# Optimization experiments

Hardware: AMD Instinct MI355X
Metric: run time of the kernel (lower is better)

## Reference

```python
import jax, jax.numpy as jnp
import numpy as np

B, S, D, H = 2, 2048, 512, 8
DH = D // H


def layer_norm(x, w, b, eps=1e-5):
    mu = x.mean(-1, keepdims=True)
    var = x.var(-1, keepdims=True)  # biased, matches nn.LayerNorm
    return (x - mu) / jnp.sqrt(var + eps) * w + b


def map_norm(qk, eps=1e-5):
    # torch.var default is unbiased (ddof=1)
    mu = qk.mean(-1, keepdims=True)
    var = qk.var(-1, ddof=1, keepdims=True)
    return (qk - mu) / jnp.sqrt(var + eps)


def sinmax(x):
    s = 1.0 + jnp.sin(10.0 * x)
    return s / s.sum(-1, keepdims=True)


def setup_inputs() -> dict:
    key = jax.random.key(0)
    ks = jax.random.split(key, 8)
    sc = 0.02
    return {
        "x": jax.random.normal(ks[0], (B, S, D), jnp.float32),
        "norm_w": jnp.ones((D,), jnp.float32),
        "norm_b": jnp.zeros((D,), jnp.float32),
        "qvk_w": jax.random.normal(ks[1], (D, 3 * D), jnp.float32) * sc,
        "qvk_b": jnp.zeros((3 * D,), jnp.float32),
        "concat_w": jax.random.normal(ks[2], (D, D), jnp.float32) * sc,
        "concat_b": jnp.zeros((D,), jnp.float32),
        "mlp_norm_w": jnp.ones((D,), jnp.float32),
        "mlp_norm_b": jnp.zeros((D,), jnp.float32),
        "mlp1_w": jax.random.normal(ks[3], (D, 2 * D), jnp.float32) * sc,
        "mlp1_b": jnp.zeros((2 * D,), jnp.float32),
        "mlp2_w": jax.random.normal(ks[4], (2 * D, D), jnp.float32) * sc,
        "mlp2_b": jnp.zeros((D,), jnp.float32),
    }


def reference(x, norm_w, norm_b, qvk_w, qvk_b, concat_w, concat_b,
              mlp_norm_w, mlp_norm_b, mlp1_w, mlp1_b, mlp2_w, mlp2_b):
    res = x
    xn = layer_norm(x, norm_w, norm_b)
    qvk = jax.nn.relu(xn @ qvk_w + qvk_b)                      # [B,S,3D]
    Q, K, V = qvk[..., :D], qvk[..., D:2 * D], qvk[..., 2 * D:]
    # contiguous d_per_head chunks per head == reshape to [B,S,H,DH]
    q = Q.reshape(B, S, H, DH).transpose(0, 2, 1, 3)           # [B,H,S,DH]
    k = K.reshape(B, S, H, DH).transpose(0, 2, 1, 3)
    v = V.reshape(B, S, H, DH).transpose(0, 2, 1, 3)
    qk = jnp.einsum('bhqd,bhkd->bhqk', q, k)                   # [B,H,S,S]
    qk = map_norm(qk)                                          # norm_ variant
    scores = sinmax(qk / np.sqrt(DH))                          # sinmax variant
    hv = jnp.einsum('bhqk,bhkd->bhqd', scores, v)
    attout = hv.transpose(0, 2, 1, 3).reshape(B, S, D)
    attout = attout @ concat_w + concat_b + res
    res_mlp = attout
    a = layer_norm(attout, mlp_norm_w, mlp_norm_b)
    h = jax.nn.gelu(a @ mlp1_w + mlp1_b, approximate=False)
    mlpout = h @ mlp2_w + mlp2_b
    return (mlpout + res_mlp, scores)
```

## Files before the change

### kernel.cpp

```cpp
#include <hip/hip_runtime.h>

#define Bb_ 2
#define S_ 2048
#define D_ 512
#define H_ 8
#define DH_ 64

typedef __attribute__((ext_vector_type(8))) __bf16 bf16x8;
typedef __attribute__((ext_vector_type(4))) __bf16 bf16x4;
typedef __attribute__((ext_vector_type(2))) __bf16 bf16x2;
typedef __attribute__((ext_vector_type(4))) float f32x4;
typedef __attribute__((ext_vector_type(8))) short short8;
typedef __attribute__((ext_vector_type(4))) unsigned u32x4;
typedef __attribute__((ext_vector_type(2))) unsigned u32x2;

__device__ __forceinline__ void gload_lds16(const void* g, void* l) {
  __builtin_amdgcn_global_load_lds(
      (const __attribute__((address_space(1))) unsigned int*)g,
      (__attribute__((address_space(3))) unsigned int*)l, 16, 0, 0);
}

__global__ __launch_bounds__(256) void wtrans_all(
    const float* __restrict__ qvk_w, const float* __restrict__ concat_w,
    const float* __restrict__ mlp1_w, const float* __restrict__ mlp2_w,
    __bf16* __restrict__ qvk_wT, __bf16* __restrict__ concat_wT,
    __bf16* __restrict__ mlp1_wT, __bf16* __restrict__ mlp2_wT) {
  int b = blockIdx.x;
  const float* w;
  __bf16* wt;
  int K, N, idx0;
  if (b < 3072) { w = qvk_w; wt = qvk_wT; K = 512; N = 1536; idx0 = b * 256; }
  else if (b < 4096) { w = concat_w; wt = concat_wT; K = 512; N = 512; idx0 = (b - 3072) * 256; }
  else if (b < 6144) { w = mlp1_w; wt = mlp1_wT; K = 512; N = 1024; idx0 = (b - 4096) * 256; }
  else { w = mlp2_w; wt = mlp2_wT; K = 1024; N = 512; idx0 = (b - 6144) * 256; }
  int idx = idx0 + threadIdx.x;
  int k = idx / N, n = idx - k * N;
  wt[(long)n * K + k] = (__bf16)w[idx];
}

__global__ __launch_bounds__(256) void ln_kernel(const float* __restrict__ x,
                                                 const float* __restrict__ w,
                                                 const float* __restrict__ b,
                                                 __bf16* __restrict__ out) {
  long row = blockIdx.x;
  const float* xr = x + row * 512;
  int t = threadIdx.x;
  float2 v = *reinterpret_cast<const float2*>(xr + t * 2);
  float s = v.x + v.y;
  float sq = v.x * v.x + v.y * v.y;
#pragma unroll
  for (int m = 1; m < 64; m <<= 1) {
    s += __shfl_xor(s, m);
    sq += __shfl_xor(sq, m);
  }
  __shared__ float red[8];
  int wid = t >> 6;
  if ((t & 63) == 0) { red[wid] = s; red[wid + 4] = sq; }
  __syncthreads();
  s = red[0] + red[1] + red[2] + red[3];
  sq = red[4] + red[5] + red[6] + red[7];
  float mu = s * (1.f / 512.f);
  float var = sq * (1.f / 512.f) - mu * mu;
  float rs = rsqrtf(var + 1e-5f);
  int c = t * 2;
  float o0 = (v.x - mu) * rs * w[c] + b[c];
  float o1 = (v.y - mu) * rs * w[c + 1] + b[c + 1];
  bf16x2 ov;
  ov[0] = (__bf16)o0;
  ov[1] = (__bf16)o1;
  *reinterpret_cast<bf16x2*>(out + row * 512 + c) = ov;
}

template <int ACT, int OUTMODE, bool HASRES>
__global__ __launch_bounds__(256) void gemm_kernel(
    const __bf16* __restrict__ A, const __bf16* __restrict__ Bt,
    const float* __restrict__ bias, const float* __restrict__ res,
    float* __restrict__ outF, __bf16* __restrict__ outB,
    __bf16* __restrict__ outK, __bf16* __restrict__ outVt,
    int lda, int ldb, int ldc, int K) {
  __shared__ __align__(16) __bf16 smem[128 * 128];
  __bf16* As = smem;
  __bf16* Bs = smem + 128 * 64;
  int t = threadIdx.x, lane = t & 63, wid = t >> 6;
  const __bf16* Ab = A + (long)blockIdx.y * 128 * lda;
  const __bf16* Bb = Bt + (long)blockIdx.x * 128 * ldb;

  f32x4 acc[4][4];
#pragma unroll
  for (int i = 0; i < 4; i++)
#pragma unroll
    for (int j = 0; j < 4; j++) acc[i][j] = (f32x4){0.f, 0.f, 0.f, 0.f};

  int wr = wid >> 1, wc = wid & 1;
  int kq = lane >> 4;
  int cbase = wid * 256;

  for (int k0 = 0; k0 < K; k0 += 64) {
    __syncthreads();
#pragma unroll
    for (int j = 0; j < 4; j++) {
      int ci = cbase + j * 64 + lane;
      int row = ci >> 3;
      int c = ci & 7;
      int sc = c ^ (row & 7);
      gload_lds16(Ab + (long)row * lda + k0 + sc * 8, &As[(cbase + j * 64) * 8]);
      gload_lds16(Bb + (long)row * ldb + k0 + sc * 8, &Bs[(cbase + j * 64) * 8]);
    }
    __syncthreads();
#pragma unroll
    for (int ks = 0; ks < 2; ks++) {
      bf16x8 af[4], bfr[4];
#pragma unroll
      for (int fm = 0; fm < 4; fm++) {
        int r = wr * 64 + fm * 16 + (lane & 15);
        int c = (ks * 4 + kq) ^ (r & 7);
        af[fm] = *reinterpret_cast<const bf16x8*>(&As[r * 64 + c * 8]);
      }
#pragma unroll
      for (int fn = 0; fn < 4; fn++) {
        int r = wc * 64 + fn * 16 + (lane & 15);
        int c = (ks * 4 + kq) ^ (r & 7);
        bfr[fn] = *reinterpret_cast<const bf16x8*>(&Bs[r * 64 + c * 8]);
      }
#pragma unroll
      for (int fm = 0; fm < 4; fm++)
#pragma unroll
        for (int fn = 0; fn < 4; fn++)
          acc[fm][fn] = __builtin_amdgcn_mfma_f32_16x16x32_bf16(af[fm], bfr[fn],
                                                                acc[fm][fn], 0, 0, 0);
    }
  }

  if (OUTMODE == 2) {
    __syncthreads();
    char* Cb = reinterpret_cast<char*>(smem);
#pragma unroll
    for (int fm = 0; fm < 4; fm++)
#pragma unroll
      for (int fn = 0; fn < 4; fn++) {
        int c = wc * 64 + fn * 16 + (lane & 15);
        int gcol = blockIdx.x * 128 + c;
        float bv = bias[gcol];
#pragma unroll
        for (int r4 = 0; r4 < 4; r4++) {
          int r = wr * 64 + fm * 16 + kq * 4 + r4;
          float v = fmaxf(acc[fm][fn][r4] + bv, 0.f);
          *reinterpret_cast<__bf16*>(Cb + r * 256 + (((c >> 3) ^ (r & 7)) << 4) +
                                     ((c & 7) << 1)) = (__bf16)v;
        }
      }
    __syncthreads();
    long bbq = (blockIdx.y * 128) >> 11;
    int srow0 = (blockIdx.y * 128) & 2047;
    if (blockIdx.x < 8) {
      int r = t >> 1, half = t & 1;
      int gcol = blockIdx.x * 128 + half * 64;
      __bf16* dst;
      if (gcol < 512)
        dst = outB + ((bbq * 8 + (gcol >> 6)) * 2048 + srow0 + r) * 64;
      else
        dst = outK + ((bbq * 8 + ((gcol - 512) >> 6)) * 2048 + srow0 + r) * 64;
      const char* srcrow = Cb + r * 256;
#pragma unroll
      for (int j = 0; j < 8; j++) {
        bf16x8 vv = *reinterpret_cast<const bf16x8*>(
            srcrow + ((((half * 8 + j) ^ (r & 7))) << 4));
        *reinterpret_cast<bf16x8*>(dst + j * 8) = vv;
      }
    } else {
      int d = t & 63, seg = t >> 6;
      int srow = srow0 + seg * 32;
#pragma unroll
      for (int h2 = 0; h2 < 2; h2++) {
        int c = h2 * 64 + d;
        int h = (blockIdx.x * 128 - 1024 + h2 * 64) >> 6;
        __bf16* dst = outVt + (bbq * 8 + h) * 131072 + (srow >> 5) * 2048 + d * 32;
        bf16x8 wv8[4];
#pragma unroll
        for (int i = 0; i < 32; i++) {
          int r = seg * 32 + i;
          __bf16 val = *reinterpret_cast<const __bf16*>(
              Cb + r * 256 + (((c >> 3) ^ (r & 7)) << 4) + ((c & 7) << 1));
          wv8[i >> 3][i & 7] = val;
        }
#pragma unroll
        for (int i4 = 0; i4 < 4; i4++)
          *reinterpret_cast<bf16x8*>(dst + i4 * 8) = wv8[i4];
      }
    }
    return;
  }

  long gr0 = (long)blockIdx.y * 128 + wr * 64;
  long gc0 = (long)blockIdx.x * 128 + wc * 64;
#pragma unroll
  for (int fm = 0; fm < 4; fm++)
#pragma unroll
    for (int fn = 0; fn < 4; fn++) {
      int col = (int)gc0 + fn * 16 + (lane & 15);
      long rbase = gr0 + fm * 16 + kq * 4;
      float bv = bias ? bias[col] : 0.f;
#pragma unroll
      for (int r4 = 0; r4 < 4; r4++) {
        long grow = rbase + r4;
        float v = acc[fm][fn][r4] + bv;
        if (HASRES) v += res[grow * ldc + col];
        if (ACT == 1) v = fmaxf(v, 0.f);
        if (ACT == 2) v = 0.5f * v * (1.f + erff(v * 0.70710678118f));
        if (OUTMODE == 0) {
          outF[grow * ldc + col] = v;
        } else {
          outB[grow * ldc + col] = (__bf16)v;
        }
      }
    }
}

__global__ __launch_bounds__(256) void gram_kernel(const __bf16* __restrict__ Kh,
                                                   float* __restrict__ gpart,
                                                   float* __restrict__ kpart) {
  int head = blockIdx.x >> 5, chunk = blockIdx.x & 31;
  __shared__ __align__(16) __bf16 kl[64 * 64];
  int t = threadIdx.x;
  const __bf16* src = Kh + ((long)head * 2048 + chunk * 64) * 64;
#pragma unroll
  for (int i = 0; i < 2; i++) {
    int e = (i * 256 + t) * 8;
    *reinterpret_cast<short8*>(&kl[e]) = *reinterpret_cast<const short8*>(&src[e]);
  }
  __syncthreads();
  int d1 = t & 63, g = t >> 6;
  float acc[16];
#pragma unroll
  for (int i = 0; i < 16; i++) acc[i] = 0.f;
  float kb = 0.f;
  for (int r = 0; r < 64; r++) {
    float k1 = (float)kl[r * 64 + d1];
    kb += k1;
    bf16x8 a = *reinterpret_cast<const bf16x8*>(&kl[r * 64 + g * 16]);
    bf16x8 b = *reinterpret_cast<const bf16x8*>(&kl[r * 64 + g * 16 + 8]);
#pragma unroll
    for (int i = 0; i < 8; i++) acc[i] += k1 * (float)a[i];
#pragma unroll
    for (int i = 0; i < 8; i++) acc[8 + i] += k1 * (float)b[i];
  }
  float* gp = gpart + ((long)chunk * 16 + head) * 4096 + d1 * 64 + g * 16;
#pragma unroll
  for (int i = 0; i < 16; i++) gp[i] = acc[i];
  if (g == 0) kpart[(chunk * 16 + head) * 64 + d1] = kb;
}

__global__ __launch_bounds__(256) void greduce_kernel(const float* __restrict__ gpart,
                                                      const float* __restrict__ kpart,
                                                      float* __restrict__ G,
                                                      float* __restrict__ kbar) {
  int idx = blockIdx.x * 256 + threadIdx.x;
  if (idx < 65536) {
    int head = idx >> 12, e = idx & 4095;
    float s = 0.f;
#pragma unroll 4
    for (int c = 0; c < 32; c++) s += gpart[((long)c * 16 + head) * 4096 + e];
    G[idx] = s;
  } else if (idx < 66560) {
    int k = idx - 65536;
    int head = k >> 6, d = k & 63;
    float s = 0.f;
#pragma unroll 4
    for (int c = 0; c < 32; c++) s += kpart[(c * 16 + head) * 64 + d];
    kbar[k] = s * (1.f / 2048.f);
  }
}

__global__ __launch_bounds__(256, 4) void stats_kernel(const __bf16* __restrict__ Qh,
                                                       const float* __restrict__ G,
                                                       const float* __restrict__ kbar,
                                                       float2* __restrict__ stats) {
  int head = blockIdx.x >> 5, sub = blockIdx.x & 31;
  __shared__ float Gl[4096];
  __shared__ float kbl[64];
  __shared__ __align__(16) float qlf[64 * 68];
  int t = threadIdx.x;
  const float* Gsrc = G + head * 4096;
#pragma unroll
  for (int i = 0; i < 4; i++) {
    int e = (i * 256 + t) * 4;
    *reinterpret_cast<float4*>(&Gl[e]) = *reinterpret_cast<const float4*>(&Gsrc[e]);
  }
  if (t < 16)
    *reinterpret_cast<float4*>(&kbl[t * 4]) =
        *reinterpret_cast<const float4*>(&kbar[head * 64 + t * 4]);
  const __bf16* qsrc = Qh + ((long)head * 2048 + sub * 64) * 64;
#pragma unroll
  for (int i = 0; i < 2; i++) {
    int e = (i * 256 + t) * 8;
    bf16x8 v = *reinterpret_cast<const bf16x8*>(&qsrc[e]);
    int row = e >> 6, col = e & 63;
    float* dst = &qlf[row * 68 + col];
#pragma unroll
    for (int j = 0; j < 8; j++) dst[j] = (float)v[j];
  }
  __syncthreads();
  int qrow = t >> 2, qt = t & 3;
  const float* qr = &qlf[qrow * 68];
  float mup = 0.f, s2p = 0.f;
#pragma unroll
  for (int i = 0; i < 16; i++) {
    int d1 = qt * 16 + i;
    const float* Gr = &Gl[d1 * 64];
    float acc = 0.f;
#pragma unroll
    for (int j = 0; j < 64; j++) acc += Gr[j] * qr[j];
    float q1 = qr[d1];
    s2p += q1 * acc;
    mup += q1 * kbl[d1];
  }
  mup += __shfl_xor(mup, 1); mup += __shfl_xor(mup, 2);
  s2p += __shfl_xor(s2p, 1); s2p += __shfl_xor(s2p, 2);
  if (qt == 0) {
    float mu = mup;
    float var = (s2p - 2048.f * mu * mu) * (1.f / 2047.f);
    stats[(head << 11) + sub * 64 + qrow] = make_float2(mu, rsqrtf(var + 1e-5f));
  }
}

__global__ __launch_bounds__(256) void attn6_kernel(
    const __bf16* __restrict__ Qh, const __bf16* __restrict__ Kh,
    const __bf16* __restrict__ Vp, const float2* __restrict__ stats,
    float* __restrict__ sco, __bf16* __restrict__ hv) {
  __shared__ __align__(16) __bf16 Ks[128 * 64];
  __shared__ __align__(16) __bf16 Vs[4 * 64 * 32];

  int bid = blockIdx.x;
  int xcd = bid & 7, j = bid >> 3;
  int head = xcd * 2 + (j >> 5);
  int qt = j & 31;
  int bb = head >> 3, hh = head & 7;
  int q0 = qt * 64;

  int t = threadIdx.x, lane = t & 63, wv = t >> 6;
  int cg = lane >> 4, ln = lane & 15;
  int sw7 = ln & 7, sw3 = ln & 3;

  int qrow = q0 + wv * 16 + ln;
  const __bf16* Qr = Qh + ((long)head * 2048 + qrow) * 64;
  bf16x8 qf0 = *reinterpret_cast<const bf16x8*>(Qr + cg * 8);
  bf16x8 qf1 = *reinterpret_cast<const bf16x8*>(Qr + 32 + cg * 8);
  float2 st = stats[(head << 11) + qrow];
  float mu = st.x, rs = st.y;

  const __bf16* Kbase = Kh + (long)head * 131072;
  const __bf16* Vbase = Vp + (long)head * 131072;

  float Z = 0.f;
  for (int kt = 0; kt < 16; kt++) {
    __syncthreads();
    const __bf16* Kt = Kbase + kt * 8192;
#pragma unroll
    for (int jj = 0; jj < 4; jj++) {
      int ci = wv * 256 + jj * 64 + lane;
      int row = ci >> 3, c = ci & 7, sc = c ^ (row & 7);
      gload_lds16(Kt + row * 64 + sc * 8, &Ks[(wv * 256 + jj * 64) * 8]);
    }
    __syncthreads();
#pragma unroll
    for (int sl = 0; sl < 8; sl++) {
      const __bf16* kr = &Ks[(sl * 16 + ln) * 64];
      bf16x8 a0 = *reinterpret_cast<const bf16x8*>(kr + ((cg ^ sw7) * 8));
      bf16x8 a1 = *reinterpret_cast<const bf16x8*>(kr + (((cg + 4) ^ sw7) * 8));
      f32x4 d = (f32x4){0.f, 0.f, 0.f, 0.f};
      d = __builtin_amdgcn_mfma_f32_16x16x32_bf16(a0, qf0, d, 0, 0, 0);
      d = __builtin_amdgcn_mfma_f32_16x16x32_bf16(a1, qf1, d, 0, 0, 0);
      Z += (1.f + __sinf(1.25f * (d[0] - mu) * rs));
      Z += (1.f + __sinf(1.25f * (d[1] - mu) * rs));
      Z += (1.f + __sinf(1.25f * (d[2] - mu) * rs));
      Z += (1.f + __sinf(1.25f * (d[3] - mu) * rs));
    }
  }
  Z += __shfl_xor(Z, 16);
  Z += __shfl_xor(Z, 32);
  float invZ = 1.f / Z;

  f32x4 hacc[4];
#pragma unroll
  for (int dt = 0; dt < 4; dt++) hacc[dt] = (f32x4){0.f, 0.f, 0.f, 0.f};
  float* srow = sco + ((long)head * 2048 + qrow) * 2048;

  for (int kt = 0; kt < 16; kt++) {
    __syncthreads();
    const __bf16* Kt = Kbase + kt * 8192;
    const __bf16* Vt = Vbase + kt * 8192;
#pragma unroll
    for (int jj = 0; jj < 4; jj++) {
      int ci = wv * 256 + jj * 64 + lane;
      int rowk = ci >> 3, ck = ci & 7, sck = ck ^ (rowk & 7);
      gload_lds16(Kt + rowk * 64 + sck * 8, &Ks[(wv * 256 + jj * 64) * 8]);
      int rowv = ci >> 2, cv = ci & 3, scv = cv ^ (rowv & 3);
      gload_lds16(Vt + rowv * 32 + scv * 8, &Vs[(wv * 256 + jj * 64) * 8]);
    }
    __syncthreads();
#pragma unroll
    for (int w = 0; w < 4; w++) {
      const __bf16* kr0 = &Ks[(w * 32 + ln) * 64];
      const __bf16* kr1 = &Ks[(w * 32 + 16 + ln) * 64];
      f32x4 d0 = (f32x4){0.f, 0.f, 0.f, 0.f}, d1 = (f32x4){0.f, 0.f, 0.f, 0.f};
      d0 = __builtin_amdgcn_mfma_f32_16x16x32_bf16(
          *reinterpret_cast<const bf16x8*>(kr0 + ((cg ^ sw7) * 8)), qf0, d0, 0, 0, 0);
      d0 = __builtin_amdgcn_mfma_f32_16x16x32_bf16(
          *reinterpret_cast<const bf16x8*>(kr0 + (((cg + 4) ^ sw7) * 8)), qf1, d0, 0, 0, 0);
      d1 = __builtin_amdgcn_mfma_f32_16x16x32_bf16(
          *reinterpret_cast<const bf16x8*>(kr1 + ((cg ^ sw7) * 8)), qf0, d1, 0, 0, 0);
      d1 = __builtin_amdgcn_mfma_f32_16x16x32_bf16(
          *reinterpret_cast<const bf16x8*>(kr1 + (((cg + 4) ^ sw7) * 8)), qf1, d1, 0, 0, 0);
      float p0 = 1.f + __sinf(1.25f * (d0[0] - mu) * rs);
      float p1 = 1.f + __sinf(1.25f * (d0[1] - mu) * rs);
      float p2 = 1.f + __sinf(1.25f * (d0[2] - mu) * rs);
      float p3 = 1.f + __sinf(1.25f * (d0[3] - mu) * rs);
      float p4 = 1.f + __sinf(1.25f * (d1[0] - mu) * rs);
      float p5 = 1.f + __sinf(1.25f * (d1[1] - mu) * rs);
      float p6 = 1.f + __sinf(1.25f * (d1[2] - mu) * rs);
      float p7 = 1.f + __sinf(1.25f * (d1[3] - mu) * rs);
      f32x4 o0 = (f32x4){p0 * invZ, p1 * invZ, p2 * invZ, p3 * invZ};
      f32x4 o1 = (f32x4){p4 * invZ, p5 * invZ, p6 * invZ, p7 * invZ};
      *reinterpret_cast<f32x4*>(srow + kt * 128 + w * 32 + cg * 4) = o0;
      *reinterpret_cast<f32x4*>(srow + kt * 128 + w * 32 + 16 + cg * 4) = o1;
      bf16x2 c0, c1, c2, c3;
      c0[0] = (__bf16)p0; c0[1] = (__bf16)p1;
      c1[0] = (__bf16)p2; c1[1] = (__bf16)p3;
      c2[0] = (__bf16)p4; c2[1] = (__bf16)p5;
      c3[0] = (__bf16)p6; c3[1] = (__bf16)p7;
      u32x4 pk = (u32x4){__builtin_bit_cast(unsigned, c0), __builtin_bit_cast(unsigned, c1),
                         __builtin_bit_cast(unsigned, c2), __builtin_bit_cast(unsigned, c3)};
      bf16x8 pf = __builtin_bit_cast(bf16x8, pk);
#pragma unroll
      for (int dt = 0; dt < 4; dt++) {
        const char* vr = reinterpret_cast<const char*>(Vs) + (w * 64 + dt * 16 + ln) * 64;
        int b0 = ((((cg >> 1) ^ sw3)) << 4) + ((cg & 1) << 3);
        int b1 = (((((cg >> 1) + 2) ^ sw3)) << 4) + ((cg & 1) << 3);
        u32x2 vlo = *reinterpret_cast<const u32x2*>(vr + b0);
        u32x2 vhi = *reinterpret_cast<const u32x2*>(vr + b1);
        u32x4 vpk = (u32x4){vlo[0], vlo[1], vhi[0], vhi[1]};
        bf16x8 vf = __builtin_bit_cast(bf16x8, vpk);
        hacc[dt] = __builtin_amdgcn_mfma_f32_16x16x32_bf16(vf, pf, hacc[dt], 0, 0, 0);
      }
    }
  }

  {
    __bf16* hq = hv + ((long)(bb * 2048) + qrow) * 512 + hh * 64;
#pragma unroll
    for (int dt = 0; dt < 4; dt++) {
      bf16x2 w0, w1;
      w0[0] = (__bf16)(hacc[dt][0] * invZ);
      w0[1] = (__bf16)(hacc[dt][1] * invZ);
      w1[0] = (__bf16)(hacc[dt][2] * invZ);
      w1[1] = (__bf16)(hacc[dt][3] * invZ);
      *reinterpret_cast<bf16x2*>(hq + dt * 16 + cg * 4) = w0;
      *reinterpret_cast<bf16x2*>(hq + dt * 16 + cg * 4 + 2) = w1;
    }
  }
}

extern "C" void kernel_launch(void* const* d_in, const int* in_sizes, int n_in,
                              void* d_out, int out_size, void* d_ws, size_t ws_size,
                              hipStream_t stream) {
  const float* x = (const float*)d_in[0];
  const float* norm_w = (const float*)d_in[1];
  const float* norm_b = (const float*)d_in[2];
  const float* qvk_w = (const float*)d_in[3];
  const float* qvk_b = (const float*)d_in[4];
  const float* concat_w = (const float*)d_in[5];
  const float* concat_b = (const float*)d_in[6];
  const float* mlp_norm_w = (const float*)d_in[7];
  const float* mlp_norm_b = (const float*)d_in[8];
  const float* mlp1_w = (const float*)d_in[9];
  const float* mlp1_b = (const float*)d_in[10];
  const float* mlp2_w = (const float*)d_in[11];
  const float* mlp2_b = (const float*)d_in[12];

  char* ws = (char*)d_ws;
  __bf16* qvk_wT = (__bf16*)(ws + 0);
  __bf16* concat_wT = (__bf16*)(ws + 1572864);
  __bf16* mlp1_wT = (__bf16*)(ws + 2097152);
  __bf16* mlp2_wT = (__bf16*)(ws + 3145728);
  __bf16* xn = (__bf16*)(ws + 4194304);
  __bf16* Qh = (__bf16*)(ws + 8388608);
  __bf16* Kh = (__bf16*)(ws + 12582912);
  __bf16* Vp = (__bf16*)(ws + 16777216);
  __bf16* hv = (__bf16*)(ws + 20971520);
  float* gpart = (float*)(ws + 25165824);
  float* attout = (float*)(ws + 25165824);
  float* kpart = (float*)(ws + 33554432);
  float* G = (float*)(ws + 33685504);
  float* kbar = (float*)(ws + 33947648);
  float2* stats = (float2*)(ws + 33951744);
  __bf16* a_b = (__bf16*)(ws + 33554432);
  __bf16* h_b = (__bf16*)(ws + 37748736);

  float* out0 = (float*)d_out;
  float* sco = out0 + 2097152;

  wtrans_all<<<8192, 256, 0, stream>>>(qvk_w, concat_w, mlp1_w, mlp2_w,
                                       qvk_wT, concat_wT, mlp1_wT, mlp2_wT);

  ln_kernel<<<4096, 256, 0, stream>>>(x, norm_w, norm_b, xn);

  gemm_kernel<1, 2, false><<<dim3(12, 32), 256, 0, stream>>>(
      xn, qvk_wT, qvk_b, nullptr, nullptr, Qh, Kh, Vp, 512, 512, 1536, 512);

  gram_kernel<<<512, 256, 0, stream>>>(Kh, gpart, kpart);
  greduce_kernel<<<260, 256, 0, stream>>>(gpart, kpart, G, kbar);
  stats_kernel<<<512, 256, 0, stream>>>(Qh, G, kbar, stats);

  attn6_kernel<<<512, 256, 0, stream>>>(Qh, Kh, Vp, stats, sco, hv);

  gemm_kernel<0, 0, true><<<dim3(4, 32), 256, 0, stream>>>(
      hv, concat_wT, concat_b, x, attout, nullptr, nullptr, nullptr, 512, 512, 512, 512);

  ln_kernel<<<4096, 256, 0, stream>>>(attout, mlp_norm_w, mlp_norm_b, a_b);

  gemm_kernel<2, 1, false><<<dim3(8, 32), 256, 0, stream>>>(
      a_b, mlp1_wT, mlp1_b, nullptr, nullptr, h_b, nullptr, nullptr, 512, 512, 1024, 512);

  gemm_kernel<0, 0, true><<<dim3(4, 32), 256, 0, stream>>>(
      h_b, mlp2_wT, mlp2_b, attout, out0, nullptr, nullptr, nullptr, 1024, 1024, 512, 1024);
}
```

Measured before the change: 222.2 us.

## Tile weight transpose through LDS and halve GEMM row tile for small GEMMs

The weight transpose/convert kernel now stages 64x64 tiles in shared memory, reading float4 rows and writing bf16x8 columns, instead of one strided scalar store per thread. The concat, MLP1 and MLP2 GEMMs are templated on a 64-row tile with a 1x4 wave layout, doubling their block count so more CUs get work on these small problems. In exchange each block reuses each B tile across fewer rows of A.

```diff
diff --git a/kernel.cpp b/kernel.cpp
--- a/kernel.cpp
+++ b/kernel.cpp
@@ -20,22 +20,42 @@
       (__attribute__((address_space(3))) unsigned int*)l, 16, 0, 0);
 }
 
-__global__ __launch_bounds__(256) void wtrans_all(
+__global__ __launch_bounds__(256) void wtrans_tile(
     const float* __restrict__ qvk_w, const float* __restrict__ concat_w,
     const float* __restrict__ mlp1_w, const float* __restrict__ mlp2_w,
     __bf16* __restrict__ qvk_wT, __bf16* __restrict__ concat_wT,
     __bf16* __restrict__ mlp1_wT, __bf16* __restrict__ mlp2_wT) {
+  __shared__ __align__(16) __bf16 tl[64 * 72];
   int b = blockIdx.x;
   const float* w;
   __bf16* wt;
-  int K, N, idx0;
-  if (b < 3072) { w = qvk_w; wt = qvk_wT; K = 512; N = 1536; idx0 = b * 256; }
-  else if (b < 4096) { w = concat_w; wt = concat_wT; K = 512; N = 512; idx0 = (b - 3072) * 256; }
-  else if (b < 6144) { w = mlp1_w; wt = mlp1_wT; K = 512; N = 1024; idx0 = (b - 4096) * 256; }
-  else { w = mlp2_w; wt = mlp2_wT; K = 1024; N = 512; idx0 = (b - 6144) * 256; }
-  int idx = idx0 + threadIdx.x;
-  int k = idx / N, n = idx - k * N;
-  wt[(long)n * K + k] = (__bf16)w[idx];
+  int K, N, rel, TN;
+  if (b < 192)      { w = qvk_w;    wt = qvk_wT;    K = 512;  N = 1536; rel = b;       TN = 24; }
+  else if (b < 256) { w = concat_w; wt = concat_wT; K = 512;  N = 512;  rel = b - 192; TN = 8;  }
+  else if (b < 384) { w = mlp1_w;   wt = mlp1_wT;   K = 512;  N = 1024; rel = b - 256; TN = 16; }
+  else              { w = mlp2_w;   wt = mlp2_wT;   K = 1024; N = 512;  rel = b - 384; TN = 8;  }
+  int tk = rel / TN, tn = rel % TN;
+  int k0 = tk * 64, n0 = tn * 64;
+  int t = threadIdx.x;
+#pragma unroll
+  for (int i = 0; i < 4; i++) {
+    int idx = i * 256 + t;
+    int kk = idx >> 4, c4 = idx & 15;
+    float4 v = *reinterpret_cast<const float4*>(w + (long)(k0 + kk) * N + n0 + c4 * 4);
+    int nb = c4 * 4;
+    tl[(nb + 0) * 72 + kk] = (__bf16)v.x;
+    tl[(nb + 1) * 72 + kk] = (__bf16)v.y;
+    tl[(nb + 2) * 72 + kk] = (__bf16)v.z;
+    tl[(nb + 3) * 72 + kk] = (__bf16)v.w;
+  }
+  __syncthreads();
+#pragma unroll
+  for (int i = 0; i < 2; i++) {
+    int idx = i * 256 + t;
+    int nn = idx >> 3, kc = idx & 7;
+    bf16x8 vv = *reinterpret_cast<const bf16x8*>(&tl[nn * 72 + kc * 8]);
+    *reinterpret_cast<bf16x8*>(wt + (long)(n0 + nn) * K + k0 + kc * 8) = vv;
+  }
 }
 
 __global__ __launch_bounds__(256) void ln_kernel(const float* __restrict__ x,
@@ -71,45 +91,50 @@
   *reinterpret_cast<bf16x2*>(out + row * 512 + c) = ov;
 }
 
-template <int ACT, int OUTMODE, bool HASRES>
+template <int ACT, int OUTMODE, bool HASRES, int BM>
 __global__ __launch_bounds__(256) void gemm_kernel(
     const __bf16* __restrict__ A, const __bf16* __restrict__ Bt,
     const float* __restrict__ bias, const float* __restrict__ res,
     float* __restrict__ outF, __bf16* __restrict__ outB,
     __bf16* __restrict__ outK, __bf16* __restrict__ outVt,
     int lda, int ldb, int ldc, int K) {
-  __shared__ __align__(16) __bf16 smem[128 * 128];
+  __shared__ __align__(16) __bf16 smem[BM * 64 + 128 * 64];
   __bf16* As = smem;
-  __bf16* Bs = smem + 128 * 64;
+  __bf16* Bs = smem + BM * 64;
   int t = threadIdx.x, lane = t & 63, wid = t >> 6;
-  const __bf16* Ab = A + (long)blockIdx.y * 128 * lda;
+  const __bf16* Ab = A + (long)blockIdx.y * BM * lda;
   const __bf16* Bb = Bt + (long)blockIdx.x * 128 * ldb;
 
-  f32x4 acc[4][4];
+  constexpr int WM = (BM == 128) ? 2 : 1;
+  constexpr int FN = (BM == 128) ? 4 : 2;
+  int wr = (WM == 2) ? (wid >> 1) : 0;
+  int wc = (WM == 2) ? (wid & 1) : wid;
+  int kq = lane >> 4;
+
+  f32x4 acc[4][FN];
 #pragma unroll
   for (int i = 0; i < 4; i++)
 #pragma unroll
-    for (int j = 0; j < 4; j++) acc[i][j] = (f32x4){0.f, 0.f, 0.f, 0.f};
-
-  int wr = wid >> 1, wc = wid & 1;
-  int kq = lane >> 4;
-  int cbase = wid * 256;
+    for (int j = 0; j < FN; j++) acc[i][j] = (f32x4){0.f, 0.f, 0.f, 0.f};
 
   for (int k0 = 0; k0 < K; k0 += 64) {
     __syncthreads();
 #pragma unroll
+    for (int j = 0; j < BM / 32; j++) {
+      int ci = wid * (BM * 2) + j * 64 + lane;
+      int row = ci >> 3, c = ci & 7, sc = c ^ (row & 7);
+      gload_lds16(Ab + (long)row * lda + k0 + sc * 8, &As[(wid * (BM * 2) + j * 64) * 8]);
+    }
+#pragma unroll
     for (int j = 0; j < 4; j++) {
-      int ci = cbase + j * 64 + lane;
-      int row = ci >> 3;
-      int c = ci & 7;
-      int sc = c ^ (row & 7);
-      gload_lds16(Ab + (long)row * lda + k0 + sc * 8, &As[(cbase + j * 64) * 8]);
-      gload_lds16(Bb + (long)row * ldb + k0 + sc * 8, &Bs[(cbase + j * 64) * 8]);
+      int ci = wid * 256 + j * 64 + lane;
+      int row = ci >> 3, c = ci & 7, sc = c ^ (row & 7);
+      gload_lds16(Bb + (long)row * ldb + k0 + sc * 8, &Bs[(wid * 256 + j * 64) * 8]);
     }
     __syncthreads();
 #pragma unroll
     for (int ks = 0; ks < 2; ks++) {
-      bf16x8 af[4], bfr[4];
+      bf16x8 af[4], bfr[FN];
 #pragma unroll
       for (int fm = 0; fm < 4; fm++) {
         int r = wr * 64 + fm * 16 + (lane & 15);
@@ -117,27 +142,27 @@
         af[fm] = *reinterpret_cast<const bf16x8*>(&As[r * 64 + c * 8]);
       }
 #pragma unroll
-      for (int fn = 0; fn < 4; fn++) {
-        int r = wc * 64 + fn * 16 + (lane & 15);
+      for (int fn = 0; fn < FN; fn++) {
+        int r = wc * (16 * FN) + fn * 16 + (lane & 15);
         int c = (ks * 4 + kq) ^ (r & 7);
         bfr[fn] = *reinterpret_cast<const bf16x8*>(&Bs[r * 64 + c * 8]);
       }
 #pragma unroll
       for (int fm = 0; fm < 4; fm++)
 #pragma unroll
-        for (int fn = 0; fn < 4; fn++)
+        for (int fn = 0; fn < FN; fn++)
           acc[fm][fn] = __builtin_amdgcn_mfma_f32_16x16x32_bf16(af[fm], bfr[fn],
                                                                 acc[fm][fn], 0, 0, 0);
     }
   }
 
-  if (OUTMODE == 2) {
+  if constexpr (OUTMODE == 2) {
     __syncthreads();
     char* Cb = reinterpret_cast<char*>(smem);
 #pragma unroll
     for (int fm = 0; fm < 4; fm++)
 #pragma unroll
-      for (int fn = 0; fn < 4; fn++) {
+      for (int fn = 0; fn < FN; fn++) {
         int c = wc * 64 + fn * 16 + (lane & 15);
         int gcol = blockIdx.x * 128 + c;
         float bv = bias[gcol];
@@ -189,31 +214,31 @@
       }
     }
     return;
-  }
-
-  long gr0 = (long)blockIdx.y * 128 + wr * 64;
-  long gc0 = (long)blockIdx.x * 128 + wc * 64;
-#pragma unroll
-  for (int fm = 0; fm < 4; fm++)
-#pragma unroll
-    for (int fn = 0; fn < 4; fn++) {
-      int col = (int)gc0 + fn * 16 + (lane & 15);
-      long rbase = gr0 + fm * 16 + kq * 4;
-      float bv = bias ? bias[col] : 0.f;
-#pragma unroll
-      for (int r4 = 0; r4 < 4; r4++) {
-        long grow = rbase + r4;
-        float v = acc[fm][fn][r4] + bv;
-        if (HASRES) v += res[grow * ldc + col];
-        if (ACT == 1) v = fmaxf(v, 0.f);
-        if (ACT == 2) v = 0.5f * v * (1.f + erff(v * 0.70710678118f));
-        if (OUTMODE == 0) {
-          outF[grow * ldc + col] = v;
-        } else {
-          outB[grow * ldc + col] = (__bf16)v;
+  } else {
+    long gr0 = (long)blockIdx.y * BM + wr * 64;
+    long gc0 = (long)blockIdx.x * 128 + wc * (16 * FN);
+#pragma unroll
+    for (int fm = 0; fm < 4; fm++)
+#pragma unroll
+      for (int fn = 0; fn < FN; fn++) {
+        int col = (int)gc0 + fn * 16 + (lane & 15);
+        long rbase = gr0 + fm * 16 + kq * 4;
+        float bv = bias ? bias[col] : 0.f;
+#pragma unroll
+        for (int r4 = 0; r4 < 4; r4++) {
+          long grow = rbase + r4;
+          float v = acc[fm][fn][r4] + bv;
+          if (HASRES) v += res[grow * ldc + col];
+          if (ACT == 1) v = fmaxf(v, 0.f);
+          if (ACT == 2) v = 0.5f * v * (1.f + erff(v * 0.70710678118f));
+          if (OUTMODE == 0) {
+            outF[grow * ldc + col] = v;
+          } else {
+            outB[grow * ldc + col] = (__bf16)v;
+          }
         }
       }
-    }
+  }
 }
 
 __global__ __launch_bounds__(256) void gram_kernel(const __bf16* __restrict__ Kh,
@@ -499,12 +524,12 @@
   float* out0 = (float*)d_out;
   float* sco = out0 + 2097152;
 
-  wtrans_all<<<8192, 256, 0, stream>>>(qvk_w, concat_w, mlp1_w, mlp2_w,
+  wtrans_tile<<<512, 256, 0, stream>>>(qvk_w, concat_w, mlp1_w, mlp2_w,
                                        qvk_wT, concat_wT, mlp1_wT, mlp2_wT);
 
   ln_kernel<<<4096, 256, 0, stream>>>(x, norm_w, norm_b, xn);
 
-  gemm_kernel<1, 2, false><<<dim3(12, 32), 256, 0, stream>>>(
+  gemm_kernel<1, 2, false, 128><<<dim3(12, 32), 256, 0, stream>>>(
       xn, qvk_wT, qvk_b, nullptr, nullptr, Qh, Kh, Vp, 512, 512, 1536, 512);
 
   gram_kernel<<<512, 256, 0, stream>>>(Kh, gpart, kpart);
@@ -513,14 +538,14 @@
 
   attn6_kernel<<<512, 256, 0, stream>>>(Qh, Kh, Vp, stats, sco, hv);
 
-  gemm_kernel<0, 0, true><<<dim3(4, 32), 256, 0, stream>>>(
+  gemm_kernel<0, 0, true, 64><<<dim3(4, 64), 256, 0, stream>>>(
       hv, concat_wT, concat_b, x, attout, nullptr, nullptr, nullptr, 512, 512, 512, 512);
 
   ln_kernel<<<4096, 256, 0, stream>>>(attout, mlp_norm_w, mlp_norm_b, a_b);
 
-  gemm_kernel<2, 1, false><<<dim3(8, 32), 256, 0, stream>>>(
+  gemm_kernel<2, 1, false, 64><<<dim3(8, 64), 256, 0, stream>>>(
       a_b, mlp1_wT, mlp1_b, nullptr, nullptr, h_b, nullptr, nullptr, 512, 512, 1024, 512);
 
-  gemm_kernel<0, 0, true><<<dim3(4, 32), 256, 0, stream>>>(
+  gemm_kernel<0, 0, true, 64><<<dim3(4, 64), 256, 0, stream>>>(
       h_b, mlp2_wT, mlp2_b, attout, out0, nullptr, nullptr, nullptr, 1024, 1024, 512, 1024);
 }
```

Measured after the change: 199.5 us. -10.2%, faster.
